# Kernel tuning notes

Hardware: AMD Instinct MI355X
Metric: run time of the kernel (lower is better)

The kernel has to match this reference:

```python
import jax, jax.numpy as jnp
import numpy as np

B_, D_, L_, N_ = 2, 1536, 2048, 16


def setup_inputs() -> dict:
    key = jax.random.key(0)
    ks = jax.random.split(key, 8)
    x = jax.random.normal(ks[0], (B_, D_, L_), dtype=jnp.float32)
    delta = jax.random.normal(ks[1], (B_, D_, L_), dtype=jnp.float32)
    # A negative (as in Mamba, A = -exp(A_log)) so the recurrence is stable
    A = -(jax.random.uniform(ks[2], (D_, N_), dtype=jnp.float32) + 0.5)
    B = jax.random.normal(ks[3], (B_, N_, L_), dtype=jnp.float32)
    C = jax.random.normal(ks[4], (B_, N_, L_), dtype=jnp.float32)
    D = jax.random.normal(ks[5], (D_,), dtype=jnp.float32)
    z = jax.random.normal(ks[6], (B_, D_, L_), dtype=jnp.float32)
    delta_bias = jax.random.normal(ks[7], (D_,), dtype=jnp.float32)
    return {"x": x, "delta": delta, "A": A, "B": B, "C": C,
            "D": D, "z": z, "delta_bias": delta_bias}


def reference(x, delta, A, B, C, D, z, delta_bias):
    # delta_softplus=True path with delta_bias, variable B (bnl) and C (bnl)
    delta = jax.nn.softplus(delta + delta_bias[None, :, None])      # (b,d,l)
    deltaA = jnp.exp(jnp.einsum('bdl,dn->bdln', delta, A))          # (b,d,l,n)
    deltaB_x = jnp.einsum('bdl,bnl,bdl->bdln', delta, B, x)         # (b,d,l,n)

    # scan over the sequence axis: h = deltaA_t * h + deltaB_x_t; y = h @ C_t
    dA_t = jnp.transpose(deltaA, (2, 0, 1, 3))     # (l,b,d,n)
    dBx_t = jnp.transpose(deltaB_x, (2, 0, 1, 3))  # (l,b,d,n)
    C_t = jnp.transpose(C, (2, 0, 1))              # (l,b,n)

    def step(h, inp):
        dA_i, dBx_i, C_i = inp
        h = dA_i * h + dBx_i                       # (b,d,n)
        y = jnp.einsum('bdn,bn->bd', h, C_i)       # (b,d)
        return h, y

    h0 = jnp.zeros((x.shape[0], A.shape[0], A.shape[1]), dtype=jnp.float32)
    _, ys = jax.lax.scan(step, h0, (dA_t, dBx_t, C_t))  # ys: (l,b,d)
    y = jnp.transpose(ys, (1, 2, 0))                    # (b,d,l)

    out = y + x * D[None, :, None]                      # D skip connection
    out = out * (z * jax.nn.sigmoid(z))                 # SiLU gate
    return out
```

## Files before the change

### kernel.cpp

```cpp
#include <hip/hip_runtime.h>
#include <math.h>

#define B_  2
#define D_  1536
#define L_  2048
#define N_  16
#define NH  8
#define LC  128
#define NCHUNK (L_ / LC)
#define NCH (B_ * D_)
#define LOG2E 1.4426950408889634f
#define LN2   0.6931471805599453f

typedef float f4 __attribute__((ext_vector_type(4)));
typedef float f8 __attribute__((ext_vector_type(8)));

__device__ __forceinline__ float exp2f_(float v) { return __builtin_amdgcn_exp2f(v); }
__device__ __forceinline__ float log2f_(float v) { return __builtin_amdgcn_logf(v); }
__device__ __forceinline__ float rcpf_(float v)  { return __builtin_amdgcn_rcpf(v); }

__device__ __forceinline__ float softplus_f(float v) {
    float t = exp2f_(v * LOG2E);
    float r = LN2 * log2f_(1.0f + t);
    return (v > 20.0f) ? v : r;
}
__device__ __forceinline__ f8 splat8(float v) { f8 r = {v,v,v,v,v,v,v,v}; return r; }
__device__ __forceinline__ f8 exp2v8(f8 a) {
    f8 r;
    r[0]=exp2f_(a[0]); r[1]=exp2f_(a[1]); r[2]=exp2f_(a[2]); r[3]=exp2f_(a[3]);
    r[4]=exp2f_(a[4]); r[5]=exp2f_(a[5]); r[6]=exp2f_(a[6]); r[7]=exp2f_(a[7]);
    return r;
}
__device__ __forceinline__ float dot8(f8 a, f8 b) {
    float p0 = fmaf(a[0], b[0], a[1]*b[1]);
    float p1 = fmaf(a[2], b[2], a[3]*b[3]);
    float p2 = fmaf(a[4], b[4], a[5]*b[5]);
    float p3 = fmaf(a[6], b[6], a[7]*b[7]);
    return (p0 + p1) + (p2 + p3);
}

#define DPP_ROW_SHR(N) (0x110 + (N))
#define DPP_ROW_BCAST15 0x142
#define DPP_WAVE_SHR1   0x138
template<int CTRL, int RMASK>
__device__ __forceinline__ float updpp(float old, float v) {
    return __int_as_float(__builtin_amdgcn_update_dpp(
        __float_as_int(old), __float_as_int(v), CTRL, RMASK, 0xF, false));
}
template<int CTRL, int RMASK>
__device__ __forceinline__ float dpp0(float v) {
    return __int_as_float(__builtin_amdgcn_update_dpp(
        0, __float_as_int(v), CTRL, RMASK, 0xF, true));
}

__global__ __launch_bounds__(64, 3)
void ssm_scan_kernel(const float* __restrict__ x,
                     const float* __restrict__ delta,
                     const float* __restrict__ A,
                     const float* __restrict__ Bm,
                     const float* __restrict__ Cm,
                     const float* __restrict__ Dv,
                     const float* __restrict__ z,
                     const float* __restrict__ dbias,
                     float* __restrict__ out)
{
    const int lane = threadIdx.x;
    const int s    = lane & 31;
    const int g    = lane >> 5;
    const int ch   = blockIdx.x;
    const int b    = ch / D_;
    const int d    = ch - b * D_;

    const float bias = dbias[d];
    const float Dd   = Dv[d];

    const float* Ab = A + d * N_ + NH * g;
    f8 A2v;
    A2v[0]=Ab[0]*LOG2E; A2v[1]=Ab[1]*LOG2E; A2v[2]=Ab[2]*LOG2E; A2v[3]=Ab[3]*LOG2E;
    A2v[4]=Ab[4]*LOG2E; A2v[5]=Ab[5]*LOG2E; A2v[6]=Ab[6]*LOG2E; A2v[7]=Ab[7]*LOG2E;

    const float* Bp = Bm + (size_t)b * (N_ * L_) + (size_t)(NH * g) * L_;
    const float* Cp = Cm + (size_t)b * (N_ * L_) + (size_t)(NH * g) * L_;
    const size_t chbase = (size_t)ch * L_;

    f8 carry = splat8(0.0f);

    f4 P0_dv = *(const f4*)(delta + chbase + s * 4);
    f4 P0_xv = *(const f4*)(x     + chbase + s * 4);
    f4 P0_B0 = *(const f4*)(Bp + 0 * L_ + s * 4);
    f4 P0_B1 = *(const f4*)(Bp + 1 * L_ + s * 4);
    f4 P0_B2 = *(const f4*)(Bp + 2 * L_ + s * 4);
    f4 P0_B3 = *(const f4*)(Bp + 3 * L_ + s * 4);
    f4 P0_B4 = *(const f4*)(Bp + 4 * L_ + s * 4);
    f4 P0_B5 = *(const f4*)(Bp + 5 * L_ + s * 4);
    f4 P0_B6 = *(const f4*)(Bp + 6 * L_ + s * 4);
    f4 P0_B7 = *(const f4*)(Bp + 7 * L_ + s * 4);
    f4 P1_dv, P1_xv, P1_B0, P1_B1, P1_B2, P1_B3, P1_B4, P1_B5, P1_B6, P1_B7;

#define BODY(c, CUR, NXT) { \
    const int off  = (c) * LC + s * 4; \
     \
    const int offn = (((c) == NCHUNK - 1) ? (c) : (c) + 1) * LC + s * 4; \
     \
    NXT##_dv = *(const f4*)(delta + chbase + offn); \
    NXT##_xv = *(const f4*)(x     + chbase + offn); \
    NXT##_B0 = *(const f4*)(Bp + 0 * L_ + offn); \
    NXT##_B1 = *(const f4*)(Bp + 1 * L_ + offn); \
    NXT##_B2 = *(const f4*)(Bp + 2 * L_ + offn); \
    NXT##_B3 = *(const f4*)(Bp + 3 * L_ + offn); \
    NXT##_B4 = *(const f4*)(Bp + 4 * L_ + offn); \
    NXT##_B5 = *(const f4*)(Bp + 5 * L_ + offn); \
    NXT##_B6 = *(const f4*)(Bp + 6 * L_ + offn); \
    NXT##_B7 = *(const f4*)(Bp + 7 * L_ + offn); \
     \
    f4 zv  = *(const f4*)(z + chbase + off); \
    f4 Cv0 = *(const f4*)(Cp + 0 * L_ + off); \
    f4 Cv1 = *(const f4*)(Cp + 1 * L_ + off); \
    f4 Cv2 = *(const f4*)(Cp + 2 * L_ + off); \
    f4 Cv3 = *(const f4*)(Cp + 3 * L_ + off); \
    f4 Cv4 = *(const f4*)(Cp + 4 * L_ + off); \
    f4 Cv5 = *(const f4*)(Cp + 5 * L_ + off); \
    f4 Cv6 = *(const f4*)(Cp + 6 * L_ + off); \
    f4 Cv7 = *(const f4*)(Cp + 7 * L_ + off); \
     \
    float dt0 = softplus_f(CUR##_dv.x + bias); \
    float dt1 = softplus_f(CUR##_dv.y + bias); \
    float dt2 = softplus_f(CUR##_dv.z + bias); \
    float dt3 = softplus_f(CUR##_dv.w + bias); \
    float u0 = dt0 * CUR##_xv.x, u1 = dt1 * CUR##_xv.y; \
    float u2 = dt2 * CUR##_xv.z, u3 = dt3 * CUR##_xv.w; \
     \
    f8 e0 = exp2v8(splat8(dt0) * A2v); \
    f8 e1 = exp2v8(splat8(dt1) * A2v); \
    f8 e2 = exp2v8(splat8(dt2) * A2v); \
    f8 e3 = exp2v8(splat8(dt3) * A2v); \
     \
    f8 tB0 = {CUR##_B0.x,CUR##_B1.x,CUR##_B2.x,CUR##_B3.x,CUR##_B4.x,CUR##_B5.x,CUR##_B6.x,CUR##_B7.x}; \
    f8 tB1 = {CUR##_B0.y,CUR##_B1.y,CUR##_B2.y,CUR##_B3.y,CUR##_B4.y,CUR##_B5.y,CUR##_B6.y,CUR##_B7.y}; \
    f8 tB2 = {CUR##_B0.z,CUR##_B1.z,CUR##_B2.z,CUR##_B3.z,CUR##_B4.z,CUR##_B5.z,CUR##_B6.z,CUR##_B7.z}; \
    f8 tB3 = {CUR##_B0.w,CUR##_B1.w,CUR##_B2.w,CUR##_B3.w,CUR##_B4.w,CUR##_B5.w,CUR##_B6.w,CUR##_B7.w}; \
    f8 SC0 = {Cv0.x,Cv1.x,Cv2.x,Cv3.x,Cv4.x,Cv5.x,Cv6.x,Cv7.x}; \
    f8 SC1 = {Cv0.y,Cv1.y,Cv2.y,Cv3.y,Cv4.y,Cv5.y,Cv6.y,Cv7.y}; \
    f8 SC2 = {Cv0.z,Cv1.z,Cv2.z,Cv3.z,Cv4.z,Cv5.z,Cv6.z,Cv7.z}; \
    f8 SC3 = {Cv0.w,Cv1.w,Cv2.w,Cv3.w,Cv4.w,Cv5.w,Cv6.w,Cv7.w}; \
     \
    f8 S0v = splat8(u0) * tB0;             \
    f8 F0v = e0; \
    f8 S1v = e1 * S0v + splat8(u1) * tB1;  f8 F1v = e1 * F0v; \
    f8 S2v = e2 * S1v + splat8(u2) * tB2;  f8 F2v = e2 * F1v; \
    f8 S3v = e3 * S2v + splat8(u3) * tB3;  f8 F3v = e3 * F2v; \
     \
    SCAN_STEP_F(DPP_ROW_SHR(1)) \
    SCAN_STEP_F(DPP_ROW_SHR(2)) \
    SCAN_STEP_F(DPP_ROW_SHR(4)) \
    SCAN_STEP_F(DPP_ROW_SHR(8)) \
    SCAN_STEP_M(DPP_ROW_BCAST15, 0xA)   \
     \
    f8 h; f8 hincv; \
    _Pragma("unroll") \
    for (int i = 0; i < NH; ++i) { \
        hincv[i] = fmaf(carry[i], F3v[i], S3v[i]);           \
        float hup = dpp0<DPP_WAVE_SHR1, 0xF>(hincv[i]);      \
        h[i] = (s == 0) ? carry[i] : hup; \
        carry[i] = __shfl(hincv[i], 31, 32);                 \
    } \
     \
    f8 t0 = F0v * h + S0v;  float y0 = dot8(t0, SC0); \
    f8 t1 = F1v * h + S1v;  float y1 = dot8(t1, SC1); \
    f8 t2 = F2v * h + S2v;  float y2 = dot8(t2, SC2); \
    float y3 = dot8(hincv, SC3); \
     \
    y0 += __shfl_xor(y0, 32, 64); \
    y1 += __shfl_xor(y1, 32, 64); \
    y2 += __shfl_xor(y2, 32, 64); \
    y3 += __shfl_xor(y3, 32, 64); \
    if (g == 0) { \
        float s0 = rcpf_(1.0f + exp2f_(-zv.x * LOG2E)); \
        float s1 = rcpf_(1.0f + exp2f_(-zv.y * LOG2E)); \
        float s2 = rcpf_(1.0f + exp2f_(-zv.z * LOG2E)); \
        float s3 = rcpf_(1.0f + exp2f_(-zv.w * LOG2E)); \
        f4 ov = { (y0 + CUR##_xv.x * Dd) * (zv.x * s0), \
                  (y1 + CUR##_xv.y * Dd) * (zv.y * s1), \
                  (y2 + CUR##_xv.z * Dd) * (zv.z * s2), \
                  (y3 + CUR##_xv.w * Dd) * (zv.w * s3) }; \
        *(f4*)(out + chbase + off) = ov; \
    } \
}

#define SCAN_STEP_F(CTRL) \
    { \
        _Pragma("unroll") \
        for (int i = 0; i < NH; ++i) { \
            float Pp = updpp<CTRL, 0xF>(1.0f, F3v[i]); \
            float Sp = dpp0<CTRL, 0xF>(S3v[i]); \
            S3v[i] = fmaf(Sp, F3v[i], S3v[i]);    \
            F3v[i] = F3v[i] * Pp; \
        } \
    }
#define SCAN_STEP_M(CTRL, RMASK) \
    { \
        _Pragma("unroll") \
        for (int i = 0; i < NH; ++i) { \
            float Pp = updpp<CTRL, RMASK>(1.0f, F3v[i]); \
            float Sp = updpp<CTRL, RMASK>(0.0f, S3v[i]); \
            S3v[i] = fmaf(Sp, F3v[i], S3v[i]); \
            F3v[i] = F3v[i] * Pp; \
        } \
    }

    for (int cc = 0; cc < NCHUNK; cc += 2) {
        BODY(cc,     P0, P1)
        BODY(cc + 1, P1, P0)
    }
}

extern "C" void kernel_launch(void* const* d_in, const int* in_sizes, int n_in,
                              void* d_out, int out_size, void* d_ws, size_t ws_size,
                              hipStream_t stream) {
    const float* x     = (const float*)d_in[0];
    const float* delta = (const float*)d_in[1];
    const float* A     = (const float*)d_in[2];
    const float* Bm    = (const float*)d_in[3];
    const float* Cm    = (const float*)d_in[4];
    const float* Dv    = (const float*)d_in[5];
    const float* z     = (const float*)d_in[6];
    const float* dbias = (const float*)d_in[7];
    float* out = (float*)d_out;

    dim3 grid(NCH);
    dim3 block(64);
    ssm_scan_kernel<<<grid, block, 0, stream>>>(x, delta, A, Bm, Cm, Dv, z, dbias, out);
}
```

Before: 170.6 us.

## Split each channel's sequence across two waves with LDS carry handoff

```diff
diff --git a/kernel.cpp b/kernel.cpp
--- a/kernel.cpp
+++ b/kernel.cpp
@@ -53,7 +53,7 @@
         0, __float_as_int(v), CTRL, RMASK, 0xF, true));
 }
 
-__global__ __launch_bounds__(64, 3)
+__global__ __launch_bounds__(128, 6)
 void ssm_scan_kernel(const float* __restrict__ x,
                      const float* __restrict__ delta,
                      const float* __restrict__ A,
@@ -64,12 +64,16 @@
                      const float* __restrict__ dbias,
                      float* __restrict__ out)
 {
-    const int lane = threadIdx.x;
+    const int tid  = threadIdx.x;
+    const int lane = tid & 63;
     const int s    = lane & 31;
-    const int g    = lane >> 5;
+    const int g    = (lane >> 5) & 1;
+    const int w    = tid >> 6;
     const int ch   = blockIdx.x;
     const int b    = ch / D_;
     const int d    = ch - b * D_;
+
+    __shared__ alignas(16) float carrybuf[2][N_];
 
     const float bias = dbias[d];
     const float Dd   = Dv[d];
@@ -83,25 +87,122 @@
     const float* Cp = Cm + (size_t)b * (N_ * L_) + (size_t)(NH * g) * L_;
     const size_t chbase = (size_t)ch * L_;
 
-    f8 carry = splat8(0.0f);
-
-    f4 P0_dv = *(const f4*)(delta + chbase + s * 4);
-    f4 P0_xv = *(const f4*)(x     + chbase + s * 4);
-    f4 P0_B0 = *(const f4*)(Bp + 0 * L_ + s * 4);
-    f4 P0_B1 = *(const f4*)(Bp + 1 * L_ + s * 4);
-    f4 P0_B2 = *(const f4*)(Bp + 2 * L_ + s * 4);
-    f4 P0_B3 = *(const f4*)(Bp + 3 * L_ + s * 4);
-    f4 P0_B4 = *(const f4*)(Bp + 4 * L_ + s * 4);
-    f4 P0_B5 = *(const f4*)(Bp + 5 * L_ + s * 4);
-    f4 P0_B6 = *(const f4*)(Bp + 6 * L_ + s * 4);
-    f4 P0_B7 = *(const f4*)(Bp + 7 * L_ + s * 4);
+    const int off0 = w * LC + s * 4;
+    f4 P0_dv = *(const f4*)(delta + chbase + off0);
+    f4 P0_xv = *(const f4*)(x     + chbase + off0);
+    f4 P0_B0 = *(const f4*)(Bp + 0 * L_ + off0);
+    f4 P0_B1 = *(const f4*)(Bp + 1 * L_ + off0);
+    f4 P0_B2 = *(const f4*)(Bp + 2 * L_ + off0);
+    f4 P0_B3 = *(const f4*)(Bp + 3 * L_ + off0);
+    f4 P0_B4 = *(const f4*)(Bp + 4 * L_ + off0);
+    f4 P0_B5 = *(const f4*)(Bp + 5 * L_ + off0);
+    f4 P0_B6 = *(const f4*)(Bp + 6 * L_ + off0);
+    f4 P0_B7 = *(const f4*)(Bp + 7 * L_ + off0);
     f4 P1_dv, P1_xv, P1_B0, P1_B1, P1_B2, P1_B3, P1_B4, P1_B5, P1_B6, P1_B7;
 
-#define BODY(c, CUR, NXT) { \
-    const int off  = (c) * LC + s * 4; \
-     \
-    const int offn = (((c) == NCHUNK - 1) ? (c) : (c) + 1) * LC + s * 4; \
-     \
+#define SCAN_STEP_F(CTRL) \
+    { \
+        _Pragma("unroll") \
+        for (int i = 0; i < NH; ++i) { \
+            float Pp = updpp<CTRL, 0xF>(1.0f, F3v[i]); \
+            float Sp = dpp0<CTRL, 0xF>(S3v[i]); \
+            S3v[i] = fmaf(Sp, F3v[i], S3v[i]);    \
+            F3v[i] = F3v[i] * Pp; \
+        } \
+    }
+#define SCAN_STEP_M(CTRL, RMASK) \
+    { \
+        _Pragma("unroll") \
+        for (int i = 0; i < NH; ++i) { \
+            float Pp = updpp<CTRL, RMASK>(1.0f, F3v[i]); \
+            float Sp = updpp<CTRL, RMASK>(0.0f, S3v[i]); \
+            S3v[i] = fmaf(Sp, F3v[i], S3v[i]); \
+            F3v[i] = F3v[i] * Pp; \
+        } \
+    }
+#define FOLDCORE \
+    { \
+        _Pragma("unroll") \
+        for (int i = 0; i < NH; ++i) { \
+            hincv[i] = fmaf(cin[i], F3v[i], S3v[i]); \
+            float hup = dpp0<DPP_WAVE_SHR1, 0xF>(hincv[i]);  \
+            h[i] = (s == 0) ? cin[i] : hup;                  \
+        } \
+        if (s == 31) { \
+            f4 lo = { hincv[0], hincv[1], hincv[2], hincv[3] }; \
+            f4 hi = { hincv[4], hincv[5], hincv[6], hincv[7] }; \
+            *(f4*)&carrybuf[w][g * NH]     = lo; \
+            *(f4*)&carrybuf[w][g * NH + 4] = hi; \
+        } \
+    }
+#define LDS_CIN(SLOT) \
+    { \
+        f4 lo = *(const f4*)&carrybuf[SLOT][g * NH]; \
+        f4 hi = *(const f4*)&carrybuf[SLOT][g * NH + 4]; \
+        cin[0]=lo.x; cin[1]=lo.y; cin[2]=lo.z; cin[3]=lo.w; \
+        cin[4]=hi.x; cin[5]=hi.y; cin[6]=hi.z; cin[7]=hi.w; \
+    }
+
+#define ITER(k, CUR, NXT) { \
+    const int c   = 2 * (k) + w;                  \
+    const int off = c * LC + s * 4; \
+     \
+     \
+    f4 Cv0 = *(const f4*)(Cp + 0 * L_ + off); \
+    f4 Cv1 = *(const f4*)(Cp + 1 * L_ + off); \
+    f4 Cv2 = *(const f4*)(Cp + 2 * L_ + off); \
+    f4 Cv3 = *(const f4*)(Cp + 3 * L_ + off); \
+    f4 Cv4 = *(const f4*)(Cp + 4 * L_ + off); \
+    f4 Cv5 = *(const f4*)(Cp + 5 * L_ + off); \
+    f4 Cv6 = *(const f4*)(Cp + 6 * L_ + off); \
+    f4 Cv7 = *(const f4*)(Cp + 7 * L_ + off); \
+    float dt0 = softplus_f(CUR##_dv.x + bias); \
+    float dt1 = softplus_f(CUR##_dv.y + bias); \
+    float dt2 = softplus_f(CUR##_dv.z + bias); \
+    float dt3 = softplus_f(CUR##_dv.w + bias); \
+    float u0 = dt0 * CUR##_xv.x, u1 = dt1 * CUR##_xv.y; \
+    float u2 = dt2 * CUR##_xv.z, u3 = dt3 * CUR##_xv.w; \
+    f8 e0 = exp2v8(splat8(dt0) * A2v); \
+    f8 e1 = exp2v8(splat8(dt1) * A2v); \
+    f8 e2 = exp2v8(splat8(dt2) * A2v); \
+    f8 e3 = exp2v8(splat8(dt3) * A2v); \
+    f8 tB0 = {CUR##_B0.x,CUR##_B1.x,CUR##_B2.x,CUR##_B3.x,CUR##_B4.x,CUR##_B5.x,CUR##_B6.x,CUR##_B7.x}; \
+    f8 tB1 = {CUR##_B0.y,CUR##_B1.y,CUR##_B2.y,CUR##_B3.y,CUR##_B4.y,CUR##_B5.y,CUR##_B6.y,CUR##_B7.y}; \
+    f8 tB2 = {CUR##_B0.z,CUR##_B1.z,CUR##_B2.z,CUR##_B3.z,CUR##_B4.z,CUR##_B5.z,CUR##_B6.z,CUR##_B7.z}; \
+    f8 tB3 = {CUR##_B0.w,CUR##_B1.w,CUR##_B2.w,CUR##_B3.w,CUR##_B4.w,CUR##_B5.w,CUR##_B6.w,CUR##_B7.w}; \
+     \
+    f8 S0v = splat8(u0) * tB0;             f8 F0v = e0; \
+    f8 S1v = e1 * S0v + splat8(u1) * tB1;  f8 F1v = e1 * F0v; \
+    f8 S2v = e2 * S1v + splat8(u2) * tB2;  f8 F2v = e2 * F1v; \
+    f8 S3v = e3 * S2v + splat8(u3) * tB3;  f8 F3v = e3 * F2v; \
+     \
+    f8 SC0 = {Cv0.x,Cv1.x,Cv2.x,Cv3.x,Cv4.x,Cv5.x,Cv6.x,Cv7.x}; \
+    f8 SC1 = {Cv0.y,Cv1.y,Cv2.y,Cv3.y,Cv4.y,Cv5.y,Cv6.y,Cv7.y}; \
+    f8 SC2 = {Cv0.z,Cv1.z,Cv2.z,Cv3.z,Cv4.z,Cv5.z,Cv6.z,Cv7.z}; \
+    f8 SC3 = {Cv0.w,Cv1.w,Cv2.w,Cv3.w,Cv4.w,Cv5.w,Cv6.w,Cv7.w}; \
+    float y00 = dot8(SC0, S0v);  f8 G0 = SC0 * F0v; \
+    float y10 = dot8(SC1, S1v);  f8 G1 = SC1 * F1v; \
+    float y20 = dot8(SC2, S2v);  f8 G2 = SC2 * F2v; \
+     \
+    SCAN_STEP_F(DPP_ROW_SHR(1)) \
+    SCAN_STEP_F(DPP_ROW_SHR(2)) \
+    SCAN_STEP_F(DPP_ROW_SHR(4)) \
+    SCAN_STEP_F(DPP_ROW_SHR(8)) \
+    SCAN_STEP_M(DPP_ROW_BCAST15, 0xA) \
+     \
+    f8 cin, h, hincv; \
+    __syncthreads();                        \
+    if (w == 0) { \
+        if ((k) == 0) { cin = splat8(0.0f); } else { LDS_CIN(1) } \
+        FOLDCORE                             \
+    } \
+    __syncthreads();                        \
+    if (w == 1) { \
+        LDS_CIN(0) \
+        FOLDCORE                             \
+    } \
+     \
+    const int offn = (((k) == 7) ? c : c + 2) * LC + s * 4;   \
     NXT##_dv = *(const f4*)(delta + chbase + offn); \
     NXT##_xv = *(const f4*)(x     + chbase + offn); \
     NXT##_B0 = *(const f4*)(Bp + 0 * L_ + offn); \
@@ -112,64 +213,11 @@
     NXT##_B5 = *(const f4*)(Bp + 5 * L_ + offn); \
     NXT##_B6 = *(const f4*)(Bp + 6 * L_ + offn); \
     NXT##_B7 = *(const f4*)(Bp + 7 * L_ + offn); \
-     \
-    f4 zv  = *(const f4*)(z + chbase + off); \
-    f4 Cv0 = *(const f4*)(Cp + 0 * L_ + off); \
-    f4 Cv1 = *(const f4*)(Cp + 1 * L_ + off); \
-    f4 Cv2 = *(const f4*)(Cp + 2 * L_ + off); \
-    f4 Cv3 = *(const f4*)(Cp + 3 * L_ + off); \
-    f4 Cv4 = *(const f4*)(Cp + 4 * L_ + off); \
-    f4 Cv5 = *(const f4*)(Cp + 5 * L_ + off); \
-    f4 Cv6 = *(const f4*)(Cp + 6 * L_ + off); \
-    f4 Cv7 = *(const f4*)(Cp + 7 * L_ + off); \
-     \
-    float dt0 = softplus_f(CUR##_dv.x + bias); \
-    float dt1 = softplus_f(CUR##_dv.y + bias); \
-    float dt2 = softplus_f(CUR##_dv.z + bias); \
-    float dt3 = softplus_f(CUR##_dv.w + bias); \
-    float u0 = dt0 * CUR##_xv.x, u1 = dt1 * CUR##_xv.y; \
-    float u2 = dt2 * CUR##_xv.z, u3 = dt3 * CUR##_xv.w; \
-     \
-    f8 e0 = exp2v8(splat8(dt0) * A2v); \
-    f8 e1 = exp2v8(splat8(dt1) * A2v); \
-    f8 e2 = exp2v8(splat8(dt2) * A2v); \
-    f8 e3 = exp2v8(splat8(dt3) * A2v); \
-     \
-    f8 tB0 = {CUR##_B0.x,CUR##_B1.x,CUR##_B2.x,CUR##_B3.x,CUR##_B4.x,CUR##_B5.x,CUR##_B6.x,CUR##_B7.x}; \
-    f8 tB1 = {CUR##_B0.y,CUR##_B1.y,CUR##_B2.y,CUR##_B3.y,CUR##_B4.y,CUR##_B5.y,CUR##_B6.y,CUR##_B7.y}; \
-    f8 tB2 = {CUR##_B0.z,CUR##_B1.z,CUR##_B2.z,CUR##_B3.z,CUR##_B4.z,CUR##_B5.z,CUR##_B6.z,CUR##_B7.z}; \
-    f8 tB3 = {CUR##_B0.w,CUR##_B1.w,CUR##_B2.w,CUR##_B3.w,CUR##_B4.w,CUR##_B5.w,CUR##_B6.w,CUR##_B7.w}; \
-    f8 SC0 = {Cv0.x,Cv1.x,Cv2.x,Cv3.x,Cv4.x,Cv5.x,Cv6.x,Cv7.x}; \
-    f8 SC1 = {Cv0.y,Cv1.y,Cv2.y,Cv3.y,Cv4.y,Cv5.y,Cv6.y,Cv7.y}; \
-    f8 SC2 = {Cv0.z,Cv1.z,Cv2.z,Cv3.z,Cv4.z,Cv5.z,Cv6.z,Cv7.z}; \
-    f8 SC3 = {Cv0.w,Cv1.w,Cv2.w,Cv3.w,Cv4.w,Cv5.w,Cv6.w,Cv7.w}; \
-     \
-    f8 S0v = splat8(u0) * tB0;             \
-    f8 F0v = e0; \
-    f8 S1v = e1 * S0v + splat8(u1) * tB1;  f8 F1v = e1 * F0v; \
-    f8 S2v = e2 * S1v + splat8(u2) * tB2;  f8 F2v = e2 * F1v; \
-    f8 S3v = e3 * S2v + splat8(u3) * tB3;  f8 F3v = e3 * F2v; \
-     \
-    SCAN_STEP_F(DPP_ROW_SHR(1)) \
-    SCAN_STEP_F(DPP_ROW_SHR(2)) \
-    SCAN_STEP_F(DPP_ROW_SHR(4)) \
-    SCAN_STEP_F(DPP_ROW_SHR(8)) \
-    SCAN_STEP_M(DPP_ROW_BCAST15, 0xA)   \
-     \
-    f8 h; f8 hincv; \
-    _Pragma("unroll") \
-    for (int i = 0; i < NH; ++i) { \
-        hincv[i] = fmaf(carry[i], F3v[i], S3v[i]);           \
-        float hup = dpp0<DPP_WAVE_SHR1, 0xF>(hincv[i]);      \
-        h[i] = (s == 0) ? carry[i] : hup; \
-        carry[i] = __shfl(hincv[i], 31, 32);                 \
-    } \
-     \
-    f8 t0 = F0v * h + S0v;  float y0 = dot8(t0, SC0); \
-    f8 t1 = F1v * h + S1v;  float y1 = dot8(t1, SC1); \
-    f8 t2 = F2v * h + S2v;  float y2 = dot8(t2, SC2); \
-    float y3 = dot8(hincv, SC3); \
-     \
+    f4 zv = *(const f4*)(z + chbase + off); \
+    float y0 = y00 + dot8(G0, h); \
+    float y1 = y10 + dot8(G1, h); \
+    float y2 = y20 + dot8(G2, h); \
+    float y3 = dot8(SC3, hincv); \
     y0 += __shfl_xor(y0, 32, 64); \
     y1 += __shfl_xor(y1, 32, 64); \
     y2 += __shfl_xor(y2, 32, 64); \
@@ -187,30 +235,9 @@
     } \
 }
 
-#define SCAN_STEP_F(CTRL) \
-    { \
-        _Pragma("unroll") \
-        for (int i = 0; i < NH; ++i) { \
-            float Pp = updpp<CTRL, 0xF>(1.0f, F3v[i]); \
-            float Sp = dpp0<CTRL, 0xF>(S3v[i]); \
-            S3v[i] = fmaf(Sp, F3v[i], S3v[i]);    \
-            F3v[i] = F3v[i] * Pp; \
-        } \
-    }
-#define SCAN_STEP_M(CTRL, RMASK) \
-    { \
-        _Pragma("unroll") \
-        for (int i = 0; i < NH; ++i) { \
-            float Pp = updpp<CTRL, RMASK>(1.0f, F3v[i]); \
-            float Sp = updpp<CTRL, RMASK>(0.0f, S3v[i]); \
-            S3v[i] = fmaf(Sp, F3v[i], S3v[i]); \
-            F3v[i] = F3v[i] * Pp; \
-        } \
-    }
-
-    for (int cc = 0; cc < NCHUNK; cc += 2) {
-        BODY(cc,     P0, P1)
-        BODY(cc + 1, P1, P0)
+    for (int kk = 0; kk < 8; kk += 2) {
+        ITER(kk,     P0, P1)
+        ITER(kk + 1, P1, P0)
     }
 }
 
@@ -228,6 +255,6 @@
     float* out = (float*)d_out;
 
     dim3 grid(NCH);
-    dim3 block(64);
+    dim3 block(128);
     ssm_scan_kernel<<<grid, block, 0, stream>>>(x, delta, A, Bm, Cm, Dv, z, dbias, out);
 }
```

Measured after the change: 544.6 us. +219.2%, slower.
